# Optimization experiments

Hardware: AMD Instinct MI355X
Metric: run time of the kernel (lower is better)

Reference implementation:

```python
import jax, jax.numpy as jnp
import numpy as np


def setup_inputs() -> dict:
    key = jax.random.key(0)
    x = jax.random.normal(key, (65536, 1024), dtype=jnp.float32)
    return {"input": x}


def reference(input) -> jnp.ndarray:
    b = input.shape[0]
    real_feat, fake_feat = input[: b // 2], input[b // 2 :]
    # diag(real @ fake.T) == row-wise dot product; avoid O(b^2 d) matmul
    sim = jnp.sum(real_feat * fake_feat, axis=-1)  # [b//2]
    loss = jnp.mean((sim + 1.0) / 2.0)
    return loss
```

## Files before the change

kernel.cpp:

```cpp
#include <hip/hip_runtime.h>


__global__ __launch_bounds__(256) void dot_partial_kernel(
    const float4* __restrict__ a, const float4* __restrict__ b,
    float* __restrict__ partials, long n4) {
    long tid = (long)blockIdx.x * blockDim.x + threadIdx.x;
    long stride = (long)gridDim.x * blockDim.x;
    float acc = 0.0f;
    for (long i = tid; i < n4; i += stride) {
        float4 x = a[i];
        float4 y = b[i];
        acc += x.x * y.x + x.y * y.y + x.z * y.z + x.w * y.w;
    }
    #pragma unroll
    for (int off = 32; off > 0; off >>= 1)
        acc += __shfl_down(acc, off, 64);
    __shared__ float s[4];
    int lane = threadIdx.x & 63;
    int wave = threadIdx.x >> 6;
    if (lane == 0) s[wave] = acc;
    __syncthreads();
    if (threadIdx.x == 0) {
        float t = s[0] + s[1] + s[2] + s[3];
        partials[blockIdx.x] = t;
    }
}

__global__ __launch_bounds__(256) void finalize_kernel(
    const float* __restrict__ partials, float* __restrict__ out,
    int nblocks, float inv_count) {
    float acc = 0.0f;
    for (int i = threadIdx.x; i < nblocks; i += blockDim.x)
        acc += partials[i];
    #pragma unroll
    for (int off = 32; off > 0; off >>= 1)
        acc += __shfl_down(acc, off, 64);
    __shared__ float s[4];
    int lane = threadIdx.x & 63;
    int wave = threadIdx.x >> 6;
    if (lane == 0) s[wave] = acc;
    __syncthreads();
    if (threadIdx.x == 0) {
        float total = s[0] + s[1] + s[2] + s[3];
        out[0] = (total * inv_count + 1.0f) * 0.5f;
    }
}

extern "C" void kernel_launch(void* const* d_in, const int* in_sizes, int n_in,
                              void* d_out, int out_size, void* d_ws, size_t ws_size,
                              hipStream_t stream) {
    const float* x = (const float*)d_in[0];
    long n = (long)in_sizes[0];
    long half = n / 2;
    long n4 = half / 4;
    long rows = half / 1024;

    const float4* a = (const float4*)x;
    const float4* b = (const float4*)(x + half);
    float* partials = (float*)d_ws;

    const int BLOCK = 256;
    const int GRID = 2048;

    dot_partial_kernel<<<GRID, BLOCK, 0, stream>>>(a, b, partials, n4);
    finalize_kernel<<<1, BLOCK, 0, stream>>>(partials, (float*)d_out, GRID,
                                             1.0f / (float)rows);
}
```

Before: 48.68 us.

## Fuse final reduction via last-block atomic counter and unroll loads by four

The separate finalize kernel is folded into the main kernel: each block writes its partial, bumps an atomic counter, and the last block to finish sums all partials and writes the loss. The grid-stride loop is unrolled by four with independent accumulators so more loads are in flight per thread. A memset of the counter is added to the stream in place of the second kernel launch. This relies on threadfence ordering and still needs one extra stream operation for the memset.

New measurement: 112.3 us. 2.31x slower.

```diff
diff --git a/kernel.cpp b/kernel.cpp
--- a/kernel.cpp
+++ b/kernel.cpp
@@ -1,68 +1,86 @@
 #include <hip/hip_runtime.h>
 
 
-__global__ __launch_bounds__(256) void dot_partial_kernel(
+constexpr int BLOCK = 256;
+constexpr int GRID  = 2048;
+
+__global__ __launch_bounds__(BLOCK) void dot_fused_kernel(
     const float4* __restrict__ a, const float4* __restrict__ b,
-    float* __restrict__ partials, long n4) {
-    long tid = (long)blockIdx.x * blockDim.x + threadIdx.x;
-    long stride = (long)gridDim.x * blockDim.x;
-    float acc = 0.0f;
-    for (long i = tid; i < n4; i += stride) {
-        float4 x = a[i];
-        float4 y = b[i];
-        acc += x.x * y.x + x.y * y.y + x.z * y.z + x.w * y.w;
+    float* __restrict__ partials, unsigned int* __restrict__ counter,
+    float* __restrict__ out, long n4, float inv_count)
+{
+    const long tid    = (long)blockIdx.x * BLOCK + threadIdx.x;
+    const long stride = (long)GRID * BLOCK;
+
+    float acc0 = 0.f, acc1 = 0.f, acc2 = 0.f, acc3 = 0.f;
+    long i = tid;
+    for (; i + 3 * stride < n4; i += 4 * stride) {
+        float4 x0 = a[i];              float4 y0 = b[i];
+        float4 x1 = a[i + stride];     float4 y1 = b[i + stride];
+        float4 x2 = a[i + 2 * stride]; float4 y2 = b[i + 2 * stride];
+        float4 x3 = a[i + 3 * stride]; float4 y3 = b[i + 3 * stride];
+        acc0 += x0.x * y0.x + x0.y * y0.y + x0.z * y0.z + x0.w * y0.w;
+        acc1 += x1.x * y1.x + x1.y * y1.y + x1.z * y1.z + x1.w * y1.w;
+        acc2 += x2.x * y2.x + x2.y * y2.y + x2.z * y2.z + x2.w * y2.w;
+        acc3 += x3.x * y3.x + x3.y * y3.y + x3.z * y3.z + x3.w * y3.w;
     }
+    for (; i < n4; i += stride) {
+        float4 x = a[i]; float4 y = b[i];
+        acc0 += x.x * y.x + x.y * y.y + x.z * y.z + x.w * y.w;
+    }
+    float acc = (acc0 + acc1) + (acc2 + acc3);
+
     #pragma unroll
     for (int off = 32; off > 0; off >>= 1)
         acc += __shfl_down(acc, off, 64);
-    __shared__ float s[4];
-    int lane = threadIdx.x & 63;
-    int wave = threadIdx.x >> 6;
+
+    __shared__ float s[BLOCK / 64];
+    __shared__ bool  is_last;
+    const int lane = threadIdx.x & 63;
+    const int wave = threadIdx.x >> 6;
     if (lane == 0) s[wave] = acc;
     __syncthreads();
+
     if (threadIdx.x == 0) {
-        float t = s[0] + s[1] + s[2] + s[3];
-        partials[blockIdx.x] = t;
+        partials[blockIdx.x] = s[0] + s[1] + s[2] + s[3];
+        __threadfence();
+        unsigned int prev = atomicAdd(counter, 1u);
+        is_last = (prev == (unsigned int)(GRID - 1));
     }
-}
+    __syncthreads();
+    if (!is_last) return;
 
-__global__ __launch_bounds__(256) void finalize_kernel(
-    const float* __restrict__ partials, float* __restrict__ out,
-    int nblocks, float inv_count) {
-    float acc = 0.0f;
-    for (int i = threadIdx.x; i < nblocks; i += blockDim.x)
-        acc += partials[i];
+    __threadfence();
+    float f = 0.f;
+    #pragma unroll
+    for (int k = 0; k < GRID / BLOCK; ++k)
+        f += partials[k * BLOCK + threadIdx.x];
     #pragma unroll
     for (int off = 32; off > 0; off >>= 1)
-        acc += __shfl_down(acc, off, 64);
-    __shared__ float s[4];
-    int lane = threadIdx.x & 63;
-    int wave = threadIdx.x >> 6;
-    if (lane == 0) s[wave] = acc;
+        f += __shfl_down(f, off, 64);
+    if (lane == 0) s[wave] = f;
     __syncthreads();
-    if (threadIdx.x == 0) {
-        float total = s[0] + s[1] + s[2] + s[3];
-        out[0] = (total * inv_count + 1.0f) * 0.5f;
-    }
+    if (threadIdx.x == 0)
+        out[0] = ((s[0] + s[1] + s[2] + s[3]) * inv_count + 1.0f) * 0.5f;
 }
 
 extern "C" void kernel_launch(void* const* d_in, const int* in_sizes, int n_in,
                               void* d_out, int out_size, void* d_ws, size_t ws_size,
                               hipStream_t stream) {
     const float* x = (const float*)d_in[0];
-    long n = (long)in_sizes[0];
+    long n    = (long)in_sizes[0];
     long half = n / 2;
-    long n4 = half / 4;
+    long n4   = half / 4;
     long rows = half / 1024;
 
     const float4* a = (const float4*)x;
     const float4* b = (const float4*)(x + half);
-    float* partials = (float*)d_ws;
 
-    const int BLOCK = 256;
-    const int GRID = 2048;
+    float* partials        = (float*)d_ws;
+    unsigned int* counter  = (unsigned int*)((char*)d_ws + GRID * sizeof(float));
 
-    dot_partial_kernel<<<GRID, BLOCK, 0, stream>>>(a, b, partials, n4);
-    finalize_kernel<<<1, BLOCK, 0, stream>>>(partials, (float*)d_out, GRID,
-                                             1.0f / (float)rows);
+    hipMemsetAsync(counter, 0, sizeof(unsigned int), stream);
+
+    dot_fused_kernel<<<GRID, BLOCK, 0, stream>>>(
+        a, b, partials, counter, (float*)d_out, n4, 1.0f / (float)rows);
 }
```
